# Kernel optimization log

Hardware: AMD Instinct MI355X
Metric: run time of the kernel (lower is better)

Reference implementation:

```python
import jax, jax.numpy as jnp
import numpy as np

B, S, D = 2, 2048, 1024
FC = 4096
H = 16
EPS = 1e-5


def _layer_norm(x, g, b):
    mu = jnp.mean(x, axis=-1, keepdims=True)
    var = jnp.var(x, axis=-1, keepdims=True)
    return (x - mu) * jax.lax.rsqrt(var + EPS) * g + b


def setup_inputs() -> dict:
    key = jax.random.key(0)
    ks = jax.random.split(key, 8)
    s = 0.02
    return {
        "x": jax.random.normal(ks[0], (B, S, D), dtype=jnp.float32),
        "ln1_g": jnp.ones((D,), jnp.float32),
        "ln1_b": jnp.zeros((D,), jnp.float32),
        "w_qkv": jax.random.normal(ks[1], (D, 3 * D), dtype=jnp.float32) * s,
        "b_qkv": jnp.zeros((3 * D,), jnp.float32),
        "ln2_g": jnp.ones((D,), jnp.float32),
        "ln2_b": jnp.zeros((D,), jnp.float32),
        "w1": jax.random.normal(ks[2], (D, FC), dtype=jnp.float32) * s,
        "b1": jnp.zeros((FC,), jnp.float32),
        "w2": jax.random.normal(ks[3], (FC, D), dtype=jnp.float32) * s,
        "b2": jnp.zeros((D,), jnp.float32),
    }


def reference(x, ln1_g, ln1_b, w_qkv, b_qkv, ln2_g, ln2_b, w1, b1, w2, b2):
    # pre-LN attention block
    h = _layer_norm(x, ln1_g, ln1_b)
    qkv = h @ w_qkv + b_qkv                       # [B,S,3D]
    q, k, v = jnp.split(qkv, 3, axis=-1)
    hd = D // H
    q = q.reshape(B, S, H, hd)
    k = k.reshape(B, S, H, hd)
    v = v.reshape(B, S, H, hd)
    scale = 1.0 / jnp.sqrt(jnp.float32(hd))
    scores = jnp.einsum("bqhd,bkhd->bhqk", q, k) * scale
    a = jax.nn.softmax(scores, axis=-1)           # [B,H,S,S]
    attn = jnp.einsum("bhqk,bkhd->bqhd", a, v).reshape(B, S, D)
    attn = attn + x
    # MLP block
    h2 = _layer_norm(attn, ln2_g, ln2_b)
    m = jax.nn.relu(h2 @ w1 + b1)
    out = m @ w2 + b2 + attn
    return out
```

## Files before the change

### kernel.cpp

```cpp
#include <hip/hip_runtime.h>
#include <stdint.h>

typedef __bf16 bf16x8 __attribute__((ext_vector_type(8)));
typedef __bf16 bf16x4 __attribute__((ext_vector_type(4)));
typedef float f32x4 __attribute__((ext_vector_type(4)));

#if __has_builtin(__builtin_amdgcn_exp2f)
#define EXP2(x) __builtin_amdgcn_exp2f(x)
#else
#define EXP2(x) exp2f(x)
#endif

__device__ __forceinline__ void g2l16(const void* gp, void* lp) {
  __builtin_amdgcn_global_load_lds(
      (__attribute__((address_space(1))) void*)const_cast<void*>(gp),
      (__attribute__((address_space(3))) void*)lp, 16, 0, 0);
}

__device__ __forceinline__ uint32_t pack_bf16(float a, float b) {
  union { float f; uint32_t u; } ua, ub;
  ua.f = a; ub.f = b;
  return (ub.u & 0xFFFF0000u) | (ua.u >> 16);
}

__global__ __launch_bounds__(256) void ln_bf16(
    const float* __restrict__ in, const float* __restrict__ g,
    const float* __restrict__ b, __bf16* __restrict__ out) {
  int row = blockIdx.x;
  int t = threadIdx.x;
  const float4* rp = (const float4*)(in + (size_t)row * 1024);
  float4 v = rp[t];
  float s = v.x + v.y + v.z + v.w;
  float ss = v.x * v.x + v.y * v.y + v.z * v.z + v.w * v.w;
#pragma unroll
  for (int o = 32; o; o >>= 1) {
    s += __shfl_down(s, o, 64);
    ss += __shfl_down(ss, o, 64);
  }
  __shared__ float red[8];
  int w = t >> 6;
  if ((t & 63) == 0) { red[w] = s; red[4 + w] = ss; }
  __syncthreads();
  float S1 = red[0] + red[1] + red[2] + red[3];
  float S2 = red[4] + red[5] + red[6] + red[7];
  float mu = S1 * (1.0f / 1024.0f);
  float var = S2 * (1.0f / 1024.0f) - mu * mu;
  float rstd = rsqrtf(var + 1e-5f);
  int c = t * 4;
  float4 gv = ((const float4*)g)[t];
  float4 bv = ((const float4*)b)[t];
  __bf16* op = out + (size_t)row * 1024 + c;
  op[0] = (__bf16)((v.x - mu) * rstd * gv.x + bv.x);
  op[1] = (__bf16)((v.y - mu) * rstd * gv.y + bv.y);
  op[2] = (__bf16)((v.z - mu) * rstd * gv.z + bv.z);
  op[3] = (__bf16)((v.w - mu) * rstd * gv.w + bv.w);
}

__global__ __launch_bounds__(256) void tcast(const float* __restrict__ in,
                                             __bf16* __restrict__ out, int R,
                                             int C) {
  __shared__ float t[32][33];
  int c0 = blockIdx.x * 32, r0 = blockIdx.y * 32;
  int tx = threadIdx.x & 31, ty = threadIdx.x >> 5;
#pragma unroll
  for (int i = 0; i < 4; i++)
    t[ty + i * 8][tx] = in[(size_t)(r0 + ty + i * 8) * C + c0 + tx];
  __syncthreads();
#pragma unroll
  for (int i = 0; i < 4; i++)
    out[(size_t)(c0 + ty + i * 8) * R + r0 + tx] = (__bf16)t[tx][ty + i * 8];
}

__global__ __launch_bounds__(256) void vtrans(const __bf16* __restrict__ qkv,
                                              __bf16* __restrict__ vT) {
  __shared__ __bf16 t[64][72];
  int bh = blockIdx.y, s0 = blockIdx.x * 64;
  int tid = threadIdx.x;
  int b = bh >> 4, h = bh & 15;
  int r = tid >> 2, c = (tid & 3) * 16;
  const __bf16* src =
      qkv + (size_t)(b * 2048 + s0 + r) * 3072 + 2048 + h * 64 + c;
  *(bf16x8*)&t[r][c] = *(const bf16x8*)src;
  *(bf16x8*)&t[r][c + 8] = *(const bf16x8*)(src + 8);
  __syncthreads();
  int d = tid >> 2;
  int cs = (tid & 3) * 16;
  __bf16 tmp[16] __attribute__((aligned(16)));
#pragma unroll
  for (int u = 0; u < 16; u++) tmp[u] = t[cs + u][d];
  __bf16* dst = vT + (size_t)(bh * 64 + d) * 2048 + s0 + cs;
  *(bf16x8*)dst = *(bf16x8*)&tmp[0];
  *(bf16x8*)(dst + 8) = *(bf16x8*)&tmp[8];
}

template <int EPI>
__global__ __launch_bounds__(256, 2) void gemm_bt(
    const __bf16* __restrict__ A, const __bf16* __restrict__ BT,
    const float* __restrict__ bias, const float* __restrict__ res,
    void* __restrict__ out, int M, int N, int K, int pm, int pn, int npx) {
  __shared__ __bf16 As[256 * 32];
  __shared__ __bf16 Bs[128 * 32];
  int tid = threadIdx.x;
  int bid = blockIdx.y * gridDim.x + blockIdx.x;
  int xcd = bid & 7;
  int j = bid >> 3;
  int jm = j % pm, jn = j / pm;
  int pyi = xcd / npx, pxi = xcd % npx;
  int m0 = (pyi * pm + jm) * 256;
  int n0 = (pxi * pn + jn) * 128;
  int lane = tid & 63, w = tid >> 6;
  int wm = (w >> 1) * 128, wn = (w & 1) * 64;
  int quad = lane >> 4, lm = lane & 15;

  int kc = K / (int)gridDim.z;
  int kBeg = (int)blockIdx.z * kc;
  int kEnd = kBeg + kc;

  f32x4 acc[8][4] = {};

  int sr = tid >> 2;
  int sc = (((tid & 3) - ((tid >> 3) & 3)) & 3) * 8;
  const __bf16* aRow = A + (size_t)(m0 + sr) * K + sc;
  const __bf16* bRow = BT + (size_t)(n0 + sr) * K + sc;
  size_t step64 = (size_t)64 * K;

  for (int k0 = kBeg; k0 < kEnd; k0 += 32) {
    g2l16(aRow + k0, &As[tid * 8]);
    g2l16(aRow + step64 + k0, &As[2048 + tid * 8]);
    g2l16(aRow + 2 * step64 + k0, &As[4096 + tid * 8]);
    g2l16(aRow + 3 * step64 + k0, &As[6144 + tid * 8]);
    g2l16(bRow + k0, &Bs[tid * 8]);
    g2l16(bRow + step64 + k0, &Bs[2048 + tid * 8]);
    __syncthreads();
    bf16x8 af[8], bv[4];
#pragma unroll
    for (int i = 0; i < 8; i++) {
      int ar = wm + i * 16 + lm;
      af[i] = *(const bf16x8*)&As[ar * 32 + ((quad + (ar >> 1)) & 3) * 8];
    }
#pragma unroll
    for (int j2 = 0; j2 < 4; j2++) {
      int br = wn + j2 * 16 + lm;
      bv[j2] = *(const bf16x8*)&Bs[br * 32 + ((quad + (br >> 1)) & 3) * 8];
    }
#pragma unroll
    for (int i = 0; i < 8; i++)
#pragma unroll
      for (int j2 = 0; j2 < 4; j2++)
        acc[i][j2] =
            __builtin_amdgcn_mfma_f32_16x16x32_bf16(af[i], bv[j2], acc[i][j2], 0, 0, 0);
    __syncthreads();
  }

#pragma unroll
  for (int i = 0; i < 8; i++)
#pragma unroll
    for (int j2 = 0; j2 < 4; j2++) {
      int rg0 = m0 + wm + i * 16 + quad * 4;
      int cg = n0 + wn + j2 * 16 + lm;
      float bi = (EPI == 3) ? 0.0f : bias[cg];
#pragma unroll
      for (int r = 0; r < 4; r++) {
        int rg = rg0 + r;
        float v = acc[i][j2][r] + bi;
        if (EPI == 0 && cg < 1024) v *= 0.18033688f;
        if (EPI == 1) v = fmaxf(v, 0.0f);
        if (EPI == 2) {
          ((float*)out)[(size_t)rg * N + cg] = v + res[(size_t)rg * N + cg];
        } else if (EPI == 3) {
          ((__bf16*)out)[(size_t)blockIdx.z * M * N + (size_t)rg * N + cg] =
              (__bf16)v;
        } else {
          ((__bf16*)out)[(size_t)rg * N + cg] = (__bf16)v;
        }
      }
    }
}

__global__ __launch_bounds__(256) void reduce_mlp2(
    const __bf16* __restrict__ part, const float* __restrict__ bias,
    const float* __restrict__ res, float* __restrict__ out) {
  size_t i = ((size_t)blockIdx.x * 256 + threadIdx.x) * 8;
  const size_t plane = (size_t)4096 * 1024;
  bf16x8 p0 = *(const bf16x8*)(part + i);
  bf16x8 p1 = *(const bf16x8*)(part + plane + i);
  bf16x8 p2 = *(const bf16x8*)(part + 2 * plane + i);
  bf16x8 p3 = *(const bf16x8*)(part + 3 * plane + i);
  int n0 = (int)(i & 1023);
  float4 b0 = *(const float4*)(bias + n0);
  float4 b1 = *(const float4*)(bias + n0 + 4);
  float4 r0 = *(const float4*)(res + i);
  float4 r1 = *(const float4*)(res + i + 4);
  float4 o0, o1;
  o0.x = (float)p0[0] + (float)p1[0] + (float)p2[0] + (float)p3[0] + b0.x + r0.x;
  o0.y = (float)p0[1] + (float)p1[1] + (float)p2[1] + (float)p3[1] + b0.y + r0.y;
  o0.z = (float)p0[2] + (float)p1[2] + (float)p2[2] + (float)p3[2] + b0.z + r0.z;
  o0.w = (float)p0[3] + (float)p1[3] + (float)p2[3] + (float)p3[3] + b0.w + r0.w;
  o1.x = (float)p0[4] + (float)p1[4] + (float)p2[4] + (float)p3[4] + b1.x + r1.x;
  o1.y = (float)p0[5] + (float)p1[5] + (float)p2[5] + (float)p3[5] + b1.y + r1.y;
  o1.z = (float)p0[6] + (float)p1[6] + (float)p2[6] + (float)p3[6] + b1.z + r1.z;
  o1.w = (float)p0[7] + (float)p1[7] + (float)p2[7] + (float)p3[7] + b1.w + r1.w;
  *(float4*)(out + i) = o0;
  *(float4*)(out + i + 4) = o1;
}

__global__ __launch_bounds__(512) void attn_kernel(
    const __bf16* __restrict__ qkv, const __bf16* __restrict__ vT,
    const float* __restrict__ x, float* __restrict__ attnres) {
  int qb = blockIdx.x, h = blockIdx.y, b = blockIdx.z;
  int tid = threadIdx.x, lane = tid & 63, w = tid >> 6;
  int quad = lane >> 4, lm = lane & 15;
  int q0 = qb * 128;

  __shared__ __bf16 Qs[128 * 64];
  __shared__ __bf16 Kbuf[2][64 * 64];
  __shared__ __bf16 Vbuf[3][64 * 64];
  __shared__ __bf16 Ps[8][16 * 72];

  const __bf16* qbase = qkv + (size_t)(b * 2048) * 3072 + h * 64;
  const __bf16* kbase = qkv + (size_t)(b * 2048) * 3072 + 1024 + h * 64;
  const __bf16* vbase = vT + (size_t)((b * 16 + h) * 64) * 2048;

  int sr = tid >> 3;
  int sc = (((tid & 7) - sr) & 7) * 8;

  g2l16(qbase + (size_t)(q0 + sr) * 3072 + sc, &Qs[tid * 8]);
  g2l16(qbase + (size_t)(q0 + 64 + sr) * 3072 + sc, &Qs[4096 + tid * 8]);
  g2l16(kbase + (size_t)sr * 3072 + sc, &Kbuf[0][tid * 8]);
  g2l16(vbase + (size_t)sr * 2048 + sc, &Vbuf[0][tid * 8]);
  __syncthreads();

  int qrow = w * 16 + lm;
  bf16x8 qf0 = *(const bf16x8*)&Qs[qrow * 64 + ((quad + qrow) & 7) * 8];
  bf16x8 qf1 = *(const bf16x8*)&Qs[qrow * 64 + ((4 + quad + qrow) & 7) * 8];

  bf16x8 ones;
#pragma unroll
  for (int i = 0; i < 8; i++) ones[i] = (__bf16)1.0f;

  f32x4 acc_o[4] = {};
  f32x4 acc_s = {};

  const __bf16* kpre = kbase + (size_t)(64 + sr) * 3072 + sc;
  const __bf16* vpre = vbase + (size_t)sr * 2048 + 64 + sc;
  __bf16* pv = Vbuf[2];
  __bf16* cv = Vbuf[0];
  __bf16* nv = Vbuf[1];
  int kcur = 0;

  for (int t = 0; t < 32; ++t) {
    bf16x8 pf0 = *(const bf16x8*)&Ps[w][lm * 72 + quad * 8];
    bf16x8 pf1 = *(const bf16x8*)&Ps[w][lm * 72 + 32 + quad * 8];
    if (t < 31) {
      g2l16(kpre, &Kbuf[kcur ^ 1][tid * 8]);
      g2l16(vpre, &nv[tid * 8]);
      kpre += (size_t)64 * 3072;
      vpre += 64;
    }
    const __bf16* Ks = Kbuf[kcur];
#pragma unroll
    for (int j = 0; j < 4; j++) {
      int krow = j * 16 + lm;
      bf16x8 kf0 = *(const bf16x8*)&Ks[krow * 64 + ((quad + krow) & 7) * 8];
      bf16x8 kf1 = *(const bf16x8*)&Ks[krow * 64 + ((4 + quad + krow) & 7) * 8];
      f32x4 z = {0.0f, 0.0f, 0.0f, 0.0f};
      z = __builtin_amdgcn_mfma_f32_16x16x32_bf16(kf0, qf0, z, 0, 0, 0);
      z = __builtin_amdgcn_mfma_f32_16x16x32_bf16(kf1, qf1, z, 0, 0, 0);
      uint2 pw;
      pw.x = pack_bf16(EXP2(z[0]), EXP2(z[1]));
      pw.y = pack_bf16(EXP2(z[2]), EXP2(z[3]));
      *(uint2*)&Ps[w][lm * 72 + j * 16 + quad * 4] = pw;
    }
    if (t > 0) {
      acc_s = __builtin_amdgcn_mfma_f32_16x16x32_bf16(ones, pf0, acc_s, 0, 0, 0);
      acc_s = __builtin_amdgcn_mfma_f32_16x16x32_bf16(ones, pf1, acc_s, 0, 0, 0);
#pragma unroll
      for (int jd = 0; jd < 4; jd++) {
        int vrow = jd * 16 + lm;
        bf16x8 vf0 = *(const bf16x8*)&pv[vrow * 64 + ((quad + vrow) & 7) * 8];
        bf16x8 vf1 =
            *(const bf16x8*)&pv[vrow * 64 + ((4 + quad + vrow) & 7) * 8];
        acc_o[jd] = __builtin_amdgcn_mfma_f32_16x16x32_bf16(vf0, pf0,
                                                            acc_o[jd], 0, 0, 0);
        acc_o[jd] = __builtin_amdgcn_mfma_f32_16x16x32_bf16(vf1, pf1,
                                                            acc_o[jd], 0, 0, 0);
      }
    }
    __bf16* tmp = pv; pv = cv; cv = nv; nv = tmp;
    kcur ^= 1;
    __syncthreads();
  }

  {
    bf16x8 pf0 = *(const bf16x8*)&Ps[w][lm * 72 + quad * 8];
    bf16x8 pf1 = *(const bf16x8*)&Ps[w][lm * 72 + 32 + quad * 8];
    acc_s = __builtin_amdgcn_mfma_f32_16x16x32_bf16(ones, pf0, acc_s, 0, 0, 0);
    acc_s = __builtin_amdgcn_mfma_f32_16x16x32_bf16(ones, pf1, acc_s, 0, 0, 0);
#pragma unroll
    for (int jd = 0; jd < 4; jd++) {
      int vrow = jd * 16 + lm;
      bf16x8 vf0 = *(const bf16x8*)&pv[vrow * 64 + ((quad + vrow) & 7) * 8];
      bf16x8 vf1 = *(const bf16x8*)&pv[vrow * 64 + ((4 + quad + vrow) & 7) * 8];
      acc_o[jd] = __builtin_amdgcn_mfma_f32_16x16x32_bf16(vf0, pf0, acc_o[jd],
                                                          0, 0, 0);
      acc_o[jd] = __builtin_amdgcn_mfma_f32_16x16x32_bf16(vf1, pf1, acc_o[jd],
                                                          0, 0, 0);
    }
  }

  float inv = 1.0f / acc_s[0];

  int qg = q0 + w * 16 + lm;
  const float* xrow = x + ((size_t)(b * 2048 + qg)) * 1024 + h * 64;
  float* orow = attnres + ((size_t)(b * 2048 + qg)) * 1024 + h * 64;
#pragma unroll
  for (int jd = 0; jd < 4; jd++) {
    int d0 = jd * 16 + quad * 4;
    float4 xv = *(const float4*)(xrow + d0);
    float4 ov;
    ov.x = acc_o[jd][0] * inv + xv.x;
    ov.y = acc_o[jd][1] * inv + xv.y;
    ov.z = acc_o[jd][2] * inv + xv.z;
    ov.w = acc_o[jd][3] * inv + xv.w;
    *(float4*)(orow + d0) = ov;
  }
}

extern "C" void kernel_launch(void* const* d_in, const int* in_sizes, int n_in,
                              void* d_out, int out_size, void* d_ws,
                              size_t ws_size, hipStream_t stream) {
  const float* x = (const float*)d_in[0];
  const float* ln1_g = (const float*)d_in[1];
  const float* ln1_b = (const float*)d_in[2];
  const float* w_qkv = (const float*)d_in[3];
  const float* b_qkv = (const float*)d_in[4];
  const float* ln2_g = (const float*)d_in[5];
  const float* ln2_b = (const float*)d_in[6];
  const float* w1 = (const float*)d_in[7];
  const float* b1 = (const float*)d_in[8];
  const float* w2 = (const float*)d_in[9];
  const float* b2 = (const float*)d_in[10];
  float* out = (float*)d_out;

  char* ws = (char*)d_ws;
  size_t o = 0;
  float* attnres = (float*)(ws + o);  o += (size_t)4096 * 1024 * 4;
  __bf16* mmid = (__bf16*)(ws + o);   o += (size_t)4096 * 4096 * 2;
  __bf16* w2T = (__bf16*)(ws + o);    o += (size_t)1024 * 4096 * 2;
  size_t base2 = o;
  __bf16* h1 = (__bf16*)(ws + o);     o += (size_t)4096 * 1024 * 2;
  __bf16* wqkvT = (__bf16*)(ws + o);  o += (size_t)3072 * 1024 * 2;
  __bf16* w1T = (__bf16*)(ws + o);    o += (size_t)4096 * 1024 * 2;
  __bf16* qkvb = (__bf16*)(ws + o);   o += (size_t)4096 * 3072 * 2;
  __bf16* vTb = (__bf16*)(ws + o);    o += (size_t)32 * 64 * 2048 * 2;
  __bf16* h2 = (__bf16*)(ws + o);     o += (size_t)4096 * 1024 * 2;
  __bf16* partials = (__bf16*)(ws + base2);

  tcast<<<dim3(96, 32), 256, 0, stream>>>(w_qkv, wqkvT, 1024, 3072);
  tcast<<<dim3(128, 32), 256, 0, stream>>>(w1, w1T, 1024, 4096);
  tcast<<<dim3(32, 128), 256, 0, stream>>>(w2, w2T, 4096, 1024);

  ln_bf16<<<4096, 256, 0, stream>>>(x, ln1_g, ln1_b, h1);
  gemm_bt<0><<<dim3(24, 16), 256, 0, stream>>>(h1, wqkvT, b_qkv, nullptr, qkvb,
                                               4096, 3072, 1024, 8, 6, 4);
  vtrans<<<dim3(32, 32), 256, 0, stream>>>(qkvb, vTb);
  attn_kernel<<<dim3(16, 16, 2), 512, 0, stream>>>(qkvb, vTb, x, attnres);
  ln_bf16<<<4096, 256, 0, stream>>>(attnres, ln2_g, ln2_b, h2);
  gemm_bt<1><<<dim3(32, 16), 256, 0, stream>>>(h2, w1T, b1, nullptr, mmid, 4096,
                                               4096, 1024, 8, 8, 4);
  gemm_bt<3><<<dim3(8, 16, 4), 256, 0, stream>>>(mmid, w2T, nullptr, nullptr,
                                                 partials, 4096, 1024, 4096, 4,
                                                 4, 2);
  reduce_mlp2<<<2048, 256, 0, stream>>>(partials, b2, attnres, out);
}
```

Baseline: 314.1 us.

## Fuse V transpose into QKV GEMM epilogue and double GEMM K-tile to 64

Drops the separate vtrans kernel: the QKV GEMM epilogue now writes the V third of its output directly in transposed [b,h,d,s] layout as 4-element bf16 stores. The GEMM K step doubles from 32 to 64, with larger LDS tiles and a new 8-way XOR swizzle, halving the number of barrier pairs per K loop. This saves one launch and one read-write pass over V. The cost is more LDS per block (48KB), which may limit the two-blocks-per-CU occupancy, and scattered 8-byte V stores in the epilogue.

Result: faster. 293.4 us (-6.6%).

```diff
diff --git a/kernel.cpp b/kernel.cpp
--- a/kernel.cpp
+++ b/kernel.cpp
@@ -71,35 +71,13 @@
     out[(size_t)(c0 + ty + i * 8) * R + r0 + tx] = (__bf16)t[tx][ty + i * 8];
 }
 
-__global__ __launch_bounds__(256) void vtrans(const __bf16* __restrict__ qkv,
-                                              __bf16* __restrict__ vT) {
-  __shared__ __bf16 t[64][72];
-  int bh = blockIdx.y, s0 = blockIdx.x * 64;
-  int tid = threadIdx.x;
-  int b = bh >> 4, h = bh & 15;
-  int r = tid >> 2, c = (tid & 3) * 16;
-  const __bf16* src =
-      qkv + (size_t)(b * 2048 + s0 + r) * 3072 + 2048 + h * 64 + c;
-  *(bf16x8*)&t[r][c] = *(const bf16x8*)src;
-  *(bf16x8*)&t[r][c + 8] = *(const bf16x8*)(src + 8);
-  __syncthreads();
-  int d = tid >> 2;
-  int cs = (tid & 3) * 16;
-  __bf16 tmp[16] __attribute__((aligned(16)));
-#pragma unroll
-  for (int u = 0; u < 16; u++) tmp[u] = t[cs + u][d];
-  __bf16* dst = vT + (size_t)(bh * 64 + d) * 2048 + s0 + cs;
-  *(bf16x8*)dst = *(bf16x8*)&tmp[0];
-  *(bf16x8*)(dst + 8) = *(bf16x8*)&tmp[8];
-}
-
 template <int EPI>
 __global__ __launch_bounds__(256, 2) void gemm_bt(
     const __bf16* __restrict__ A, const __bf16* __restrict__ BT,
-    const float* __restrict__ bias, const float* __restrict__ res,
+    const float* __restrict__ bias, __bf16* __restrict__ outV,
     void* __restrict__ out, int M, int N, int K, int pm, int pn, int npx) {
-  __shared__ __bf16 As[256 * 32];
-  __shared__ __bf16 Bs[128 * 32];
+  __shared__ __bf16 As[256 * 64];
+  __shared__ __bf16 Bs[128 * 64];
   int tid = threadIdx.x;
   int bid = blockIdx.y * gridDim.x + blockIdx.x;
   int xcd = bid & 7;
@@ -118,37 +96,40 @@
 
   f32x4 acc[8][4] = {};
 
-  int sr = tid >> 2;
-  int sc = (((tid & 3) - ((tid >> 3) & 3)) & 3) * 8;
+  int sr = tid >> 3;
+  int sc = (((tid & 7) - sr) & 7) * 8;
   const __bf16* aRow = A + (size_t)(m0 + sr) * K + sc;
   const __bf16* bRow = BT + (size_t)(n0 + sr) * K + sc;
-  size_t step64 = (size_t)64 * K;
-
-  for (int k0 = kBeg; k0 < kEnd; k0 += 32) {
-    g2l16(aRow + k0, &As[tid * 8]);
-    g2l16(aRow + step64 + k0, &As[2048 + tid * 8]);
-    g2l16(aRow + 2 * step64 + k0, &As[4096 + tid * 8]);
-    g2l16(aRow + 3 * step64 + k0, &As[6144 + tid * 8]);
-    g2l16(bRow + k0, &Bs[tid * 8]);
-    g2l16(bRow + step64 + k0, &Bs[2048 + tid * 8]);
+  size_t step32 = (size_t)32 * K;
+
+  for (int k0 = kBeg; k0 < kEnd; k0 += 64) {
+#pragma unroll
+    for (int ro = 0; ro < 8; ro++)
+      g2l16(aRow + ro * step32 + k0, &As[ro * 2048 + tid * 8]);
+#pragma unroll
+    for (int ro = 0; ro < 4; ro++)
+      g2l16(bRow + ro * step32 + k0, &Bs[ro * 2048 + tid * 8]);
     __syncthreads();
-    bf16x8 af[8], bv[4];
-#pragma unroll
-    for (int i = 0; i < 8; i++) {
-      int ar = wm + i * 16 + lm;
-      af[i] = *(const bf16x8*)&As[ar * 32 + ((quad + (ar >> 1)) & 3) * 8];
-    }
-#pragma unroll
-    for (int j2 = 0; j2 < 4; j2++) {
-      int br = wn + j2 * 16 + lm;
-      bv[j2] = *(const bf16x8*)&Bs[br * 32 + ((quad + (br >> 1)) & 3) * 8];
-    }
-#pragma unroll
-    for (int i = 0; i < 8; i++)
-#pragma unroll
-      for (int j2 = 0; j2 < 4; j2++)
-        acc[i][j2] =
-            __builtin_amdgcn_mfma_f32_16x16x32_bf16(af[i], bv[j2], acc[i][j2], 0, 0, 0);
+#pragma unroll
+    for (int kk = 0; kk < 2; kk++) {
+      bf16x8 af[8], bv[4];
+#pragma unroll
+      for (int i = 0; i < 8; i++) {
+        int ar = wm + i * 16 + lm;
+        af[i] = *(const bf16x8*)&As[ar * 64 + ((kk * 4 + quad + ar) & 7) * 8];
+      }
+#pragma unroll
+      for (int j2 = 0; j2 < 4; j2++) {
+        int br = wn + j2 * 16 + lm;
+        bv[j2] = *(const bf16x8*)&Bs[br * 64 + ((kk * 4 + quad + br) & 7) * 8];
+      }
+#pragma unroll
+      for (int i = 0; i < 8; i++)
+#pragma unroll
+        for (int j2 = 0; j2 < 4; j2++)
+          acc[i][j2] = __builtin_amdgcn_mfma_f32_16x16x32_bf16(
+              af[i], bv[j2], acc[i][j2], 0, 0, 0);
+    }
     __syncthreads();
   }
 
@@ -159,15 +140,22 @@
       int rg0 = m0 + wm + i * 16 + quad * 4;
       int cg = n0 + wn + j2 * 16 + lm;
       float bi = (EPI == 3) ? 0.0f : bias[cg];
+      if (EPI == 0 && cg >= 2048) {
+        int hh = (cg - 2048) >> 6, dd = (cg - 2048) & 63;
+        int bq = rg0 >> 11, s = rg0 & 2047;
+        bf16x4 pv;
+#pragma unroll
+        for (int r = 0; r < 4; r++) pv[r] = (__bf16)(acc[i][j2][r] + bi);
+        *(bf16x4*)&outV[(size_t)((bq * 16 + hh) * 64 + dd) * 2048 + s] = pv;
+        continue;
+      }
 #pragma unroll
       for (int r = 0; r < 4; r++) {
         int rg = rg0 + r;
         float v = acc[i][j2][r] + bi;
         if (EPI == 0 && cg < 1024) v *= 0.18033688f;
         if (EPI == 1) v = fmaxf(v, 0.0f);
-        if (EPI == 2) {
-          ((float*)out)[(size_t)rg * N + cg] = v + res[(size_t)rg * N + cg];
-        } else if (EPI == 3) {
+        if (EPI == 3) {
           ((__bf16*)out)[(size_t)blockIdx.z * M * N + (size_t)rg * N + cg] =
               (__bf16)v;
         } else {
@@ -361,9 +349,8 @@
   tcast<<<dim3(32, 128), 256, 0, stream>>>(w2, w2T, 4096, 1024);
 
   ln_bf16<<<4096, 256, 0, stream>>>(x, ln1_g, ln1_b, h1);
-  gemm_bt<0><<<dim3(24, 16), 256, 0, stream>>>(h1, wqkvT, b_qkv, nullptr, qkvb,
+  gemm_bt<0><<<dim3(24, 16), 256, 0, stream>>>(h1, wqkvT, b_qkv, vTb, qkvb,
                                                4096, 3072, 1024, 8, 6, 4);
-  vtrans<<<dim3(32, 32), 256, 0, stream>>>(qkvb, vTb);
   attn_kernel<<<dim3(16, 16, 2), 512, 0, stream>>>(qkvb, vTb, x, attnres);
   ln_bf16<<<4096, 256, 0, stream>>>(attnres, ln2_g, ln2_b, h2);
   gemm_bt<1><<<dim3(32, 16), 256, 0, stream>>>(h2, w1T, b1, nullptr, mmid, 4096,
```
